# Kernel optimization log

Measured on AMD Instinct MI355X. Metric: run time of the kernel, lower is better.

The kernel has to match this reference:

```python
import jax, jax.numpy as jnp
import numpy as np

NUM_CLASSES = 32
N_ITER = 5
KNN_K = 16


def _inv_softplus(v: float) -> float:
    return float(np.log(np.expm1(v)))


def setup_inputs() -> dict:
    key = jax.random.key(0)
    k1, k2, k3 = jax.random.split(key, 3)
    B, N, C, D = 2, 4096, NUM_CLASSES, 256
    logits = jax.random.normal(k1, (B, N, C), dtype=jnp.float32)
    rois = jax.random.uniform(k2, (B, N, 6), dtype=jnp.float32)
    feats = jax.random.normal(k3, (B, N, D), dtype=jnp.float32)
    raw_sigma = jnp.asarray(_inv_softplus(4.0), dtype=jnp.float32)
    raw_smoothness = jnp.asarray(_inv_softplus(1.0), dtype=jnp.float32)
    return {
        "logits": logits,
        "rois": rois,
        "appearance_features": feats,
        "raw_sigma": raw_sigma,
        "raw_smoothness": raw_smoothness,
    }


def reference(logits, rois, appearance_features, raw_sigma, raw_smoothness):
    B, N, C = logits.shape
    # roi centers of 3D boxes: mean of (xmin,ymin,zmin) and (xmax,ymax,zmax)
    centers = (rois[:, :, :3] + rois[:, :, 3:]) * 0.5
    sq = jnp.sum(centers * centers, axis=-1)  # [B,N]
    dist_sq = jnp.maximum(
        sq[:, :, None] + sq[:, None, :]
        - 2.0 * jnp.einsum("bnd,bmd->bnm", centers, centers),
        0.0,
    )  # squared euclidean [B,N,N]

    identity = jnp.eye(N, dtype=bool)[None]  # [1,N,N]
    valid = jnp.sum(jnp.abs(rois), axis=-1) > 0  # [B,N]
    valid_pairs = valid[:, :, None] & valid[:, None, :]  # [B,N,N]

    # ---- kNN adjacency (symmetric, no self loops) ----
    k_eff = min(KNN_K, max(N - 1, 1))
    masked = jnp.where(valid_pairs & ~identity, dist_sq, jnp.inf)
    neg_topv, knn_idx = jax.lax.top_k(-masked, k_eff)  # smallest k_eff dists
    finite = jnp.isfinite(-neg_topv)  # [B,N,k]
    b_idx = jnp.arange(B)[:, None, None]
    n_idx = jnp.arange(N)[None, :, None]
    adjacency = jnp.zeros((B, N, N), dtype=bool).at[b_idx, n_idx, knn_idx].set(finite)
    adjacency = adjacency | jnp.swapaxes(adjacency, 1, 2)
    adjacency = adjacency & valid_pairs & ~identity

    sigma = jnp.maximum(jax.nn.softplus(raw_sigma), 1e-6)
    smoothness = jax.nn.softplus(raw_smoothness)

    # ---- pairwise kernel: spatial gaussian * appearance cosine affinity ----
    kernel = jnp.exp(-0.5 * dist_sq / (sigma * sigma))
    feat_norm = jnp.maximum(
        jnp.linalg.norm(appearance_features, axis=-1, keepdims=True), 1e-6
    )
    feats_n = appearance_features / feat_norm
    cosine = jnp.einsum("bnd,bmd->bnm", feats_n, feats_n)
    affinity = jnp.clip((cosine + 1.0) * 0.5, 0.0, 1.0)
    kernel = kernel * affinity
    kernel = jnp.where(identity, 0.0, kernel) * adjacency.astype(logits.dtype)
    kernel = kernel / jnp.maximum(jnp.sum(kernel, axis=-1, keepdims=True), 1e-6)

    # ---- class compatibility (normalized squared label distance) ----
    idx = jnp.arange(C, dtype=logits.dtype)
    compat = (idx[:, None] - idx[None, :]) ** 2
    compat = compat / jnp.maximum(compat.max(), 1.0)

    # ---- mean-field iterations ----
    q_probs = jax.nn.softmax(logits, axis=-1)
    refined = logits
    for _ in range(N_ITER):
        q_neighbors = jnp.einsum("bnm,bmc->bnc", kernel, q_probs)
        pairwise_term = jnp.einsum("bnc,cd->bnd", q_neighbors, compat)
        refined = logits - smoothness * pairwise_term
        q_probs = jax.nn.softmax(refined, axis=-1)
    return refined
```

## Files before the change

kernel.cpp:

```cpp
#include <hip/hip_runtime.h>
#include <math.h>

constexpr int B = 2;
constexpr int N = 4096;
constexpr int C = 32;
constexpr int D = 256;
constexpr int K = 16;
constexpr int NW = N / 32;
constexpr int CAP = 128;
constexpr int ROWS = B * N;

__device__ __forceinline__ unsigned short f2bf(float f) {
    unsigned u = __float_as_uint(f);
    return (unsigned short)((u + 0x7fffu + ((u >> 16) & 1u)) >> 16);
}
__device__ __forceinline__ float bflo(unsigned u) { return __uint_as_float(u << 16); }
__device__ __forceinline__ float bfhi(unsigned u) { return __uint_as_float(u & 0xffff0000u); }

__global__ void pre_kernel(const float* __restrict__ rois,
                           const float* __restrict__ feats,
                           float4* __restrict__ centers4,
                           unsigned short* __restrict__ fnbf,
                           uint2* __restrict__ adj_zero) {
    const int t = threadIdx.x;
    const int wid = t >> 6, lane = t & 63;
    const int r = blockIdx.x * 4 + wid;

    adj_zero[blockIdx.x * 256 + t] = make_uint2(0u, 0u);

    if (r >= ROWS) return;

    const float4* f4 = reinterpret_cast<const float4*>(feats) + (size_t)r * (D / 4);
    float4 v = f4[lane];
    float ss = v.x * v.x + v.y * v.y + v.z * v.z + v.w * v.w;
#pragma unroll
    for (int off = 32; off; off >>= 1) ss += __shfl_xor(ss, off);

    const float invn = 1.0f / fmaxf(sqrtf(ss), 1e-6f);
    unsigned u0 = (unsigned)f2bf(v.x * invn) | ((unsigned)f2bf(v.y * invn) << 16);
    unsigned u1 = (unsigned)f2bf(v.z * invn) | ((unsigned)f2bf(v.w * invn) << 16);
    *reinterpret_cast<uint2*>(fnbf + (size_t)r * D + lane * 4) = make_uint2(u0, u1);

    if (lane == 0) {
        const float* rp = rois + (size_t)r * 6;
        float a0 = rp[0], a1 = rp[1], a2 = rp[2], a3 = rp[3], a4 = rp[4], a5 = rp[5];
        float cx = (a0 + a3) * 0.5f, cy = (a1 + a4) * 0.5f, cz = (a2 + a5) * 0.5f;
        float sq = cx * cx + cy * cy + cz * cz;
        float s = fabsf(a0) + fabsf(a1) + fabsf(a2) + fabsf(a3) + fabsf(a4) + fabsf(a5);
        centers4[r] = make_float4(cx, cy, cz, (s > 0.0f) ? sq : INFINITY);
    }
}

__global__ __launch_bounds__(1024, 8) void knn_kernel(const float4* __restrict__ centers4,
                                                      unsigned* __restrict__ adj) {
    __shared__ float4 s_c[N];
    __shared__ unsigned s_pm[16][64];
    __shared__ unsigned long long s_buf[16][64];
    __shared__ int s_cnt[16];
    __shared__ float s_tau[16];

    const int t = threadIdx.x;
    const int lane = t & 63;
    const int wv = t >> 6;
    const int r0 = blockIdx.x * 16;
    const int nbase = r0 & (N - 1);
    const int gbase = r0 - nbase;

    if (t < 16) s_cnt[t] = 0;
    ((unsigned*)s_pm)[t] = 0x7F800000u;
    for (int i = t; i < N; i += 1024) s_c[i] = centers4[gbase + i];
    __syncthreads();

    float4 cmv[4];
    int    mv[4];
#pragma unroll
    for (int u = 0; u < 4; ++u) {
        mv[u] = (wv << 8) + (u << 6) + lane;
        cmv[u] = s_c[mv[u]];
    }

#pragma unroll 4
    for (int rr = 0; rr < 16; ++rr) {
        const int nrow = nbase + rr;
        const float4 rc = s_c[nrow];
        float mn = INFINITY;
#pragma unroll
        for (int u = 0; u < 4; ++u) {
            float dist = fmaxf(rc.w + cmv[u].w -
                               2.0f * (rc.x * cmv[u].x + rc.y * cmv[u].y + rc.z * cmv[u].z), 0.0f);
            mn = fminf(mn, (mv[u] == nrow) ? INFINITY : dist);
        }
        atomicMin(&s_pm[rr][lane], __float_as_uint(mn));
    }
    __syncthreads();

    {
        float v = __uint_as_float(s_pm[wv][lane]);
#pragma unroll
        for (int k = 2; k <= 64; k <<= 1) {
#pragma unroll
            for (int j = k >> 1; j > 0; j >>= 1) {
                float o = __shfl_xor(v, j);
                bool take_min = (((lane & j) == 0) == ((lane & k) == 0));
                v = take_min ? fminf(v, o) : fmaxf(v, o);
            }
        }
        if (lane == 15) s_tau[wv] = v;
    }
    __syncthreads();

#pragma unroll 4
    for (int rr = 0; rr < 16; ++rr) {
        const int nrow = nbase + rr;
        const float tau = s_tau[rr];
        const float4 rc = s_c[nrow];
#pragma unroll
        for (int u = 0; u < 4; ++u) {
            float dist = fmaxf(rc.w + cmv[u].w -
                               2.0f * (rc.x * cmv[u].x + rc.y * cmv[u].y + rc.z * cmv[u].z), 0.0f);
            if (dist <= tau && mv[u] != nrow) {
                int pos = atomicAdd(&s_cnt[rr], 1);
                if (pos < 64)
                    s_buf[rr][pos] = ((unsigned long long)__float_as_uint(dist) << 32)
                                     | (unsigned)mv[u];
            }
        }
    }
    __syncthreads();

    const int rg = r0 + wv;
    const int n = nbase + wv;
    const int cnt = s_cnt[wv];

    int my_sel = -1;
    if (cnt <= 64) {
        unsigned long long key = (lane < cnt) ? s_buf[wv][lane] : ~0ull;
#pragma unroll
        for (int k = 2; k <= 64; k <<= 1) {
#pragma unroll
            for (int j = k >> 1; j > 0; j >>= 1) {
                unsigned long long o = __shfl_xor(key, j);
                bool take_min = (((lane & j) == 0) == ((lane & k) == 0));
                unsigned long long mn = (key < o) ? key : o;
                unsigned long long mx = (key < o) ? o : key;
                key = take_min ? mn : mx;
            }
        }
        if (lane < K && key != ~0ull) my_sel = (int)(unsigned)key;
    } else {
        const float4 cq = s_c[n];
        unsigned long long removed = 0ull;
        for (int round = 0; round < K; ++round) {
            float bd = INFINITY; int bi = 0x7FFFFFFF;
            for (int j = 0; j < 64; ++j) {
                const int m = lane + (j << 6);
                float4 cm = s_c[m];
                float dist = fmaxf(cq.w + cm.w -
                                   2.0f * (cq.x * cm.x + cq.y * cm.y + cq.z * cm.z), 0.0f);
                bool skip = ((removed >> j) & 1ull) || (m == n);
                if (!skip && dist < bd) { bd = dist; bi = m; }
            }
            float md = bd;
#pragma unroll
            for (int off = 32; off; off >>= 1) md = fminf(md, __shfl_xor(md, off));
            if (md == INFINITY) break;
            int kk = (bd == md) ? bi : 0x7FFFFFFF;
#pragma unroll
            for (int off = 32; off; off >>= 1) kk = min(kk, __shfl_xor(kk, off));
            if (lane == round) my_sel = kk;
            if (kk == bi) removed |= 1ull << (bi >> 6);
        }
    }

    if (my_sel >= 0) {
        atomicOr(&adj[(size_t)rg * NW + (my_sel >> 5)], 1u << (my_sel & 31));
        atomicOr(&adj[(size_t)(gbase + my_sel) * NW + (n >> 5)], 1u << (n & 31));
    }
}

__global__ __launch_bounds__(256) void build_kernel(const unsigned short* __restrict__ fnbf,
                             const float4* __restrict__ centers4,
                             const unsigned* __restrict__ adj,
                             uint2* __restrict__ nbr,
                             int* __restrict__ nbr_cnt,
                             const float* __restrict__ raw_sigma,
                             const float* __restrict__ logits,
                             float2* __restrict__ mu0) {
    const int t = threadIdx.x;
    const int lane = t & 63;
    const int wv = t >> 6;
    const int r = blockIdx.x * 4 + wv;
    const int base = r - (r & (N - 1));

    __shared__ float4 s_q[4][16 * 5];
    __shared__ int    s_list[4][CAP];
    __shared__ float  s_w[4][CAP];

    uint2 wpair = *reinterpret_cast<const uint2*>(adj + (size_t)r * NW + 2 * lane);
    const int pc = __popc(wpair.x) + __popc(wpair.y);
    int sc = pc;
#pragma unroll
    for (int off = 1; off < 64; off <<= 1) {
        int o = __shfl_up(sc, off);
        if (lane >= off) sc += o;
    }
    const int total = __shfl(sc, 63);
    const int cnt = total > CAP ? CAP : total;
    int o = sc - pc;
    {
        unsigned ww = wpair.x; int mb = lane * 64;
        while (ww) { int b = __ffs(ww) - 1; if (o < CAP) s_list[wv][o] = mb + b; ++o; ww &= ww - 1; }
        ww = wpair.y; mb = lane * 64 + 32;
        while (ww) { int b = __ffs(ww) - 1; if (o < CAP) s_list[wv][o] = mb + b; ++o; ww &= ww - 1; }
    }

    {
        uint2 qw = *reinterpret_cast<const uint2*>(fnbf + (size_t)r * D + 4 * lane);
        float4 qv = make_float4(bflo(qw.x), bfhi(qw.x), bflo(qw.y), bfhi(qw.y));
        const int e = (lane & 31) >> 1;
        const int s = ((lane >> 5) << 1) | (lane & 1);
        s_q[wv][5 * e + s] = qv;
    }

    const float rs = raw_sigma[0];
    const float sigma = fmaxf(log1pf(expf(rs)), 1e-6f);
    const float nhalf_inv_s2 = -0.5f / (sigma * sigma);
    const float4 cq = centers4[r];
    const uint4* fn4 = reinterpret_cast<const uint4*>(fnbf);

    {
        const int g = lane >> 4;
        const int e = lane & 15;
        for (int i0 = 0; i0 < cnt; i0 += 4) {
            const int i = i0 + g;
            const bool act = (i < cnt);
            const int gm = base + s_list[wv][act ? i : 0];
            uint4 a = fn4[(size_t)gm * 32 + e];
            uint4 b = fn4[(size_t)gm * 32 + 16 + e];
            float4 cm = centers4[gm];
            float4 qa0 = s_q[wv][5 * e + 0], qa1 = s_q[wv][5 * e + 1];
            float4 qb0 = s_q[wv][5 * e + 2], qb1 = s_q[wv][5 * e + 3];
            float p = bflo(a.x) * qa0.x + bfhi(a.x) * qa0.y
                    + bflo(a.y) * qa0.z + bfhi(a.y) * qa0.w
                    + bflo(a.z) * qa1.x + bfhi(a.z) * qa1.y
                    + bflo(a.w) * qa1.z + bfhi(a.w) * qa1.w
                    + bflo(b.x) * qb0.x + bfhi(b.x) * qb0.y
                    + bflo(b.y) * qb0.z + bfhi(b.y) * qb0.w
                    + bflo(b.z) * qb1.x + bfhi(b.z) * qb1.y
                    + bflo(b.w) * qb1.z + bfhi(b.w) * qb1.w;
#pragma unroll
            for (int off = 1; off < 16; off <<= 1) p += __shfl_xor(p, off);
            float aff = fminf(fmaxf((p + 1.0f) * 0.5f, 0.0f), 1.0f);
            float dist = fmaxf(cq.w + cm.w -
                               2.0f * (cq.x * cm.x + cq.y * cm.y + cq.z * cm.z), 0.0f);
            if (e == 0 && act) s_w[wv][i] = expf(dist * nhalf_inv_s2) * aff;
        }
    }

    float ps = 0.0f;
    for (int i = lane; i < cnt; i += 64) ps += s_w[wv][i];
#pragma unroll
    for (int off = 32; off; off >>= 1) ps += __shfl_xor(ps, off);
    const float inv_sum = 1.0f / fmaxf(ps, 1e-6f);

    for (int i = lane; i < cnt; i += 64) {
        nbr[(size_t)r * CAP + i] = make_uint2((unsigned)s_list[wv][i],
                                              __float_as_uint(s_w[wv][i] * inv_sum));
    }
    if (lane == 0) nbr_cnt[r] = cnt;

    if (lane < C) {
        float x = logits[(size_t)r * C + lane];
        float mx = x;
#pragma unroll
        for (int off = 16; off; off >>= 1) mx = fmaxf(mx, __shfl_xor(mx, off, 32));
        float e = expf(x - mx);
        const float fc = (float)lane;
        float s0 = e, s1 = e * fc, s2 = e * fc * fc;
#pragma unroll
        for (int off = 16; off; off >>= 1) {
            s0 += __shfl_xor(s0, off, 32);
            s1 += __shfl_xor(s1, off, 32);
            s2 += __shfl_xor(s2, off, 32);
        }
        if (lane == 0) mu0[r] = make_float2(s1 / s0, s2 / s0);
    }
}

__global__ void iter_kernel(const float* __restrict__ logits,
                            const uint2* __restrict__ nbr,
                            const int* __restrict__ nbr_cnt,
                            const float2* __restrict__ mu_in,
                            float2* __restrict__ mu_out,
                            float* __restrict__ out,
                            const float* __restrict__ raw_smooth,
                            int last) {
    const int t = threadIdx.x;
    const int r = blockIdx.x * 8 + (t >> 5);
    const int c = t & 31;
    const int base = r - (r & (N - 1));
    const float smooth = log1pf(expf(raw_smooth[0]));

    const int cnt = nbr_cnt[r];
    const uint2* np = nbr + (size_t)r * CAP;

    float m0 = 0.0f, m1 = 0.0f, m2 = 0.0f;
    for (int j = c; j < cnt; j += 32) {
        uint2 e = np[j];
        float w = __uint_as_float(e.y);
        float2 mu = mu_in[base + (int)e.x];
        m0 += w;
        m1 += w * mu.x;
        m2 += w * mu.y;
    }
#pragma unroll
    for (int off = 16; off; off >>= 1) {
        m0 += __shfl_xor(m0, off, 32);
        m1 += __shfl_xor(m1, off, 32);
        m2 += __shfl_xor(m2, off, 32);
    }

    const float fc = (float)c;
    float pw = (m2 - 2.0f * fc * m1 + fc * fc * m0) * (1.0f / 961.0f);
    float refined = logits[(size_t)r * C + c] - smooth * pw;

    if (last) {
        out[(size_t)r * C + c] = refined;
        return;
    }

    float mx = refined;
#pragma unroll
    for (int off = 16; off; off >>= 1) mx = fmaxf(mx, __shfl_xor(mx, off, 32));
    float e = expf(refined - mx);
    float s0 = e, s1 = e * fc, s2 = e * fc * fc;
#pragma unroll
    for (int off = 16; off; off >>= 1) {
        s0 += __shfl_xor(s0, off, 32);
        s1 += __shfl_xor(s1, off, 32);
        s2 += __shfl_xor(s2, off, 32);
    }
    if (c == 0) mu_out[r] = make_float2(s1 / s0, s2 / s0);
}

extern "C" void kernel_launch(void* const* d_in, const int* in_sizes, int n_in,
                              void* d_out, int out_size, void* d_ws, size_t ws_size,
                              hipStream_t stream) {
    const float* logits     = (const float*)d_in[0];
    const float* rois       = (const float*)d_in[1];
    const float* feats      = (const float*)d_in[2];
    const float* raw_sigma  = (const float*)d_in[3];
    const float* raw_smooth = (const float*)d_in[4];
    float* out = (float*)d_out;

    char* ws = (char*)d_ws;
    size_t off = 0;
    auto alloc = [&](size_t bytes) -> void* {
        void* p = ws + off;
        off += (bytes + 255) & ~(size_t)255;
        return p;
    };
    float4*         centers4 = (float4*)        alloc((size_t)ROWS * sizeof(float4));
    unsigned short* fnbf     = (unsigned short*)alloc((size_t)ROWS * D * 2);
    unsigned*       adj      = (unsigned*)      alloc((size_t)ROWS * NW * 4);
    uint2*          nbr      = (uint2*)         alloc((size_t)ROWS * CAP * 8);
    int*            nbr_cnt  = (int*)           alloc((size_t)ROWS * 4);
    float2*         mu_a     = (float2*)        alloc((size_t)ROWS * 8);
    float2*         mu_b     = (float2*)        alloc((size_t)ROWS * 8);

    pre_kernel<<<ROWS / 4, 256, 0, stream>>>(rois, feats, centers4, fnbf, (uint2*)adj);
    knn_kernel<<<ROWS / 16, 1024, 0, stream>>>(centers4, adj);
    build_kernel<<<ROWS / 4, 256, 0, stream>>>(fnbf, centers4, adj,
                                               nbr, nbr_cnt, raw_sigma, logits, mu_a);

    float2* mi = mu_a;
    float2* mo = mu_b;
    for (int it = 0; it < 5; ++it) {
        iter_kernel<<<ROWS / 8, 256, 0, stream>>>(logits, nbr, nbr_cnt,
                                                  mi, mo, out, raw_smooth,
                                                  (it == 4) ? 1 : 0);
        float2* tmp = mi; mi = mo; mo = tmp;
    }
}
```

Measured before the change: 71.42 us.

## Fuse pairs of mean-field iterations by recomputing neighbor moments per row

New measurement: 96.44 us. 35.0% more time.

```diff
diff --git a/kernel.cpp b/kernel.cpp
--- a/kernel.cpp
+++ b/kernel.cpp
@@ -287,14 +287,108 @@
     }
 }
 
-__global__ void iter_kernel(const float* __restrict__ logits,
-                            const uint2* __restrict__ nbr,
-                            const int* __restrict__ nbr_cnt,
-                            const float2* __restrict__ mu_in,
-                            float2* __restrict__ mu_out,
-                            float* __restrict__ out,
-                            const float* __restrict__ raw_smooth,
-                            int last) {
+__global__ __launch_bounds__(256) void iter2_kernel(const float* __restrict__ logits,
+                                                    const uint2* __restrict__ nbr,
+                                                    const int* __restrict__ nbr_cnt,
+                                                    const float2* __restrict__ mu_in,
+                                                    float2* __restrict__ mu_out,
+                                                    const float* __restrict__ raw_smooth) {
+    const int t = threadIdx.x;
+    const int lane = t & 63;
+    const int wv = t >> 6;
+    const int r = blockIdx.x * 4 + wv;
+    const int base = r - (r & (N - 1));
+    const float smooth = log1pf(expf(raw_smooth[0]));
+
+    __shared__ float2 s_mu[4][CAP];
+
+    const int cnt = nbr_cnt[r];
+    const uint2* own = nbr + (size_t)r * CAP;
+
+    const int sub = lane & 1;
+    const int p = lane >> 1;
+
+    for (int i0 = 0; i0 < cnt; i0 += 32) {
+        const int i = i0 + p;
+        const bool act = (i < cnt);
+        const int gm = base + (int)own[act ? i : 0].x;
+        const int cm = act ? nbr_cnt[gm] : 0;
+        const uint2* np = nbr + (size_t)gm * CAP;
+
+        float m0 = 0.0f, m1 = 0.0f, m2 = 0.0f;
+        for (int j = sub; j < cm; j += 2) {
+            uint2 e = np[j];
+            float w = __uint_as_float(e.y);
+            float2 mu = mu_in[base + (int)e.x];
+            m0 += w; m1 += w * mu.x; m2 += w * mu.y;
+        }
+        m0 += __shfl_xor(m0, 1); m1 += __shfl_xor(m1, 1); m2 += __shfl_xor(m2, 1);
+
+        const float4* lg4 = reinterpret_cast<const float4*>(logits + (size_t)gm * C + sub * 16);
+        float4 xa = lg4[0], xb = lg4[1], xc = lg4[2], xd = lg4[3];
+        float xv[16] = { xa.x, xa.y, xa.z, xa.w, xb.x, xb.y, xb.z, xb.w,
+                         xc.x, xc.y, xc.z, xc.w, xd.x, xd.y, xd.z, xd.w };
+        float ref[16];
+        float mx = -INFINITY;
+#pragma unroll
+        for (int k = 0; k < 16; ++k) {
+            float fc = (float)(sub * 16 + k);
+            float pw = (m2 - 2.0f * fc * m1 + fc * fc * m0) * (1.0f / 961.0f);
+            float rr = xv[k] - smooth * pw;
+            ref[k] = rr;
+            mx = fmaxf(mx, rr);
+        }
+        mx = fmaxf(mx, __shfl_xor(mx, 1));
+        float s0 = 0.0f, s1 = 0.0f, s2 = 0.0f;
+#pragma unroll
+        for (int k = 0; k < 16; ++k) {
+            float fc = (float)(sub * 16 + k);
+            float e = expf(ref[k] - mx);
+            s0 += e; s1 += e * fc; s2 += e * fc * fc;
+        }
+        s0 += __shfl_xor(s0, 1); s1 += __shfl_xor(s1, 1); s2 += __shfl_xor(s2, 1);
+        if (act && sub == 0) s_mu[wv][i] = make_float2(s1 / s0, s2 / s0);
+    }
+
+    float m0 = 0.0f, m1 = 0.0f, m2 = 0.0f;
+    for (int j = lane; j < cnt; j += 64) {
+        uint2 e = own[j];
+        float w = __uint_as_float(e.y);
+        float2 mu = s_mu[wv][j];
+        m0 += w; m1 += w * mu.x; m2 += w * mu.y;
+    }
+#pragma unroll
+    for (int off = 32; off; off >>= 1) {
+        m0 += __shfl_xor(m0, off);
+        m1 += __shfl_xor(m1, off);
+        m2 += __shfl_xor(m2, off);
+    }
+
+    if (lane < C) {
+        const float fc = (float)lane;
+        float pw = (m2 - 2.0f * fc * m1 + fc * fc * m0) * (1.0f / 961.0f);
+        float refined = logits[(size_t)r * C + lane] - smooth * pw;
+        float mx = refined;
+#pragma unroll
+        for (int off = 16; off; off >>= 1) mx = fmaxf(mx, __shfl_xor(mx, off, 32));
+        float e = expf(refined - mx);
+        float s0 = e, s1 = e * fc, s2 = e * fc * fc;
+#pragma unroll
+        for (int off = 16; off; off >>= 1) {
+            s0 += __shfl_xor(s0, off, 32);
+            s1 += __shfl_xor(s1, off, 32);
+            s2 += __shfl_xor(s2, off, 32);
+        }
+        if (lane == 0) mu_out[r] = make_float2(s1 / s0, s2 / s0);
+    }
+}
+
+__global__ void iter_last_kernel(const float* __restrict__ logits,
+                                 const uint2* __restrict__ nbr,
+                                 const int* __restrict__ nbr_cnt,
+                                 const float2* __restrict__ mu_in,
+                                 float* __restrict__ out,
+                                 const float* __restrict__ raw_smooth) {
     const int t = threadIdx.x;
     const int r = blockIdx.x * 8 + (t >> 5);
     const int c = t & 31;
@@ -309,9 +403,7 @@
         uint2 e = np[j];
         float w = __uint_as_float(e.y);
         float2 mu = mu_in[base + (int)e.x];
-        m0 += w;
-        m1 += w * mu.x;
-        m2 += w * mu.y;
+        m0 += w; m1 += w * mu.x; m2 += w * mu.y;
     }
 #pragma unroll
     for (int off = 16; off; off >>= 1) {
@@ -322,25 +414,7 @@
 
     const float fc = (float)c;
     float pw = (m2 - 2.0f * fc * m1 + fc * fc * m0) * (1.0f / 961.0f);
-    float refined = logits[(size_t)r * C + c] - smooth * pw;
-
-    if (last) {
-        out[(size_t)r * C + c] = refined;
-        return;
-    }
-
-    float mx = refined;
-#pragma unroll
-    for (int off = 16; off; off >>= 1) mx = fmaxf(mx, __shfl_xor(mx, off, 32));
-    float e = expf(refined - mx);
-    float s0 = e, s1 = e * fc, s2 = e * fc * fc;
-#pragma unroll
-    for (int off = 16; off; off >>= 1) {
-        s0 += __shfl_xor(s0, off, 32);
-        s1 += __shfl_xor(s1, off, 32);
-        s2 += __shfl_xor(s2, off, 32);
-    }
-    if (c == 0) mu_out[r] = make_float2(s1 / s0, s2 / s0);
+    out[(size_t)r * C + c] = logits[(size_t)r * C + c] - smooth * pw;
 }
 
 extern "C" void kernel_launch(void* const* d_in, const int* in_sizes, int n_in,
@@ -373,12 +447,7 @@
     build_kernel<<<ROWS / 4, 256, 0, stream>>>(fnbf, centers4, adj,
                                                nbr, nbr_cnt, raw_sigma, logits, mu_a);
 
-    float2* mi = mu_a;
-    float2* mo = mu_b;
-    for (int it = 0; it < 5; ++it) {
-        iter_kernel<<<ROWS / 8, 256, 0, stream>>>(logits, nbr, nbr_cnt,
-                                                  mi, mo, out, raw_smooth,
-                                                  (it == 4) ? 1 : 0);
-        float2* tmp = mi; mi = mo; mo = tmp;
-    }
-}
+    iter2_kernel<<<ROWS / 4, 256, 0, stream>>>(logits, nbr, nbr_cnt, mu_a, mu_b, raw_smooth);
+    iter2_kernel<<<ROWS / 4, 256, 0, stream>>>(logits, nbr, nbr_cnt, mu_b, mu_a, raw_smooth);
+    iter_last_kernel<<<ROWS / 8, 256, 0, stream>>>(logits, nbr, nbr_cnt, mu_a, out, raw_smooth);
+}
```

## Fuse preprocessing into kNN kernel and replace adjacency zeroing with memset

Applied to the files above, without the earlier changes.

New measurement: 74.52 us. 4.3% more time.

```diff
diff --git a/kernel.cpp b/kernel.cpp
--- a/kernel.cpp
+++ b/kernel.cpp
@@ -17,41 +17,12 @@
 __device__ __forceinline__ float bflo(unsigned u) { return __uint_as_float(u << 16); }
 __device__ __forceinline__ float bfhi(unsigned u) { return __uint_as_float(u & 0xffff0000u); }
 
-__global__ void pre_kernel(const float* __restrict__ rois,
-                           const float* __restrict__ feats,
-                           float4* __restrict__ centers4,
-                           unsigned short* __restrict__ fnbf,
-                           uint2* __restrict__ adj_zero) {
-    const int t = threadIdx.x;
-    const int wid = t >> 6, lane = t & 63;
-    const int r = blockIdx.x * 4 + wid;
-
-    adj_zero[blockIdx.x * 256 + t] = make_uint2(0u, 0u);
-
-    if (r >= ROWS) return;
-
-    const float4* f4 = reinterpret_cast<const float4*>(feats) + (size_t)r * (D / 4);
-    float4 v = f4[lane];
-    float ss = v.x * v.x + v.y * v.y + v.z * v.z + v.w * v.w;
-#pragma unroll
-    for (int off = 32; off; off >>= 1) ss += __shfl_xor(ss, off);
-
-    const float invn = 1.0f / fmaxf(sqrtf(ss), 1e-6f);
-    unsigned u0 = (unsigned)f2bf(v.x * invn) | ((unsigned)f2bf(v.y * invn) << 16);
-    unsigned u1 = (unsigned)f2bf(v.z * invn) | ((unsigned)f2bf(v.w * invn) << 16);
-    *reinterpret_cast<uint2*>(fnbf + (size_t)r * D + lane * 4) = make_uint2(u0, u1);
-
-    if (lane == 0) {
-        const float* rp = rois + (size_t)r * 6;
-        float a0 = rp[0], a1 = rp[1], a2 = rp[2], a3 = rp[3], a4 = rp[4], a5 = rp[5];
-        float cx = (a0 + a3) * 0.5f, cy = (a1 + a4) * 0.5f, cz = (a2 + a5) * 0.5f;
-        float sq = cx * cx + cy * cy + cz * cz;
-        float s = fabsf(a0) + fabsf(a1) + fabsf(a2) + fabsf(a3) + fabsf(a4) + fabsf(a5);
-        centers4[r] = make_float4(cx, cy, cz, (s > 0.0f) ? sq : INFINITY);
-    }
-}
-
-__global__ __launch_bounds__(1024, 8) void knn_kernel(const float4* __restrict__ centers4,
+__global__ __launch_bounds__(1024, 8) void knn_kernel(const float* __restrict__ rois,
+                                                      const float* __restrict__ feats,
+                                                      const float* __restrict__ logits,
+                                                      float4* __restrict__ centers4,
+                                                      unsigned short* __restrict__ fnbf,
+                                                      float2* __restrict__ mu0,
                                                       unsigned* __restrict__ adj) {
     __shared__ float4 s_c[N];
     __shared__ unsigned s_pm[16][64];
@@ -65,10 +36,63 @@
     const int r0 = blockIdx.x * 16;
     const int nbase = r0 & (N - 1);
     const int gbase = r0 - nbase;
+    const int rg0 = r0 + wv;
 
     if (t < 16) s_cnt[t] = 0;
     ((unsigned*)s_pm)[t] = 0x7F800000u;
-    for (int i = t; i < N; i += 1024) s_c[i] = centers4[gbase + i];
+
+    {
+        const float4* f4 = reinterpret_cast<const float4*>(feats) + (size_t)rg0 * (D / 4);
+        float4 v = f4[lane];
+        float ss = v.x * v.x + v.y * v.y + v.z * v.z + v.w * v.w;
+#pragma unroll
+        for (int off = 32; off; off >>= 1) ss += __shfl_xor(ss, off);
+        const float invn = 1.0f / fmaxf(sqrtf(ss), 1e-6f);
+        unsigned u0 = (unsigned)f2bf(v.x * invn) | ((unsigned)f2bf(v.y * invn) << 16);
+        unsigned u1 = (unsigned)f2bf(v.z * invn) | ((unsigned)f2bf(v.w * invn) << 16);
+        *reinterpret_cast<uint2*>(fnbf + (size_t)rg0 * D + lane * 4) = make_uint2(u0, u1);
+
+        if (lane < C) {
+            float x = logits[(size_t)rg0 * C + lane];
+            float mx = x;
+#pragma unroll
+            for (int off = 16; off; off >>= 1) mx = fmaxf(mx, __shfl_xor(mx, off, 32));
+            float e = expf(x - mx);
+            const float fc = (float)lane;
+            float s0 = e, s1 = e * fc, s2 = e * fc * fc;
+#pragma unroll
+            for (int off = 16; off; off >>= 1) {
+                s0 += __shfl_xor(s0, off, 32);
+                s1 += __shfl_xor(s1, off, 32);
+                s2 += __shfl_xor(s2, off, 32);
+            }
+            if (lane == 0) mu0[rg0] = make_float2(s1 / s0, s2 / s0);
+        }
+
+        if (lane == 0) {
+            const float* rp = rois + (size_t)rg0 * 6;
+            float a0 = rp[0], a1 = rp[1], a2 = rp[2], a3 = rp[3], a4 = rp[4], a5 = rp[5];
+            float cx = (a0 + a3) * 0.5f, cy = (a1 + a4) * 0.5f, cz = (a2 + a5) * 0.5f;
+            float sq = cx * cx + cy * cy + cz * cz;
+            float s = fabsf(a0) + fabsf(a1) + fabsf(a2) + fabsf(a3) + fabsf(a4) + fabsf(a5);
+            centers4[rg0] = make_float4(cx, cy, cz, (s > 0.0f) ? sq : INFINITY);
+        }
+    }
+
+    {
+        const float2* rois2 = reinterpret_cast<const float2*>(rois);
+        for (int i = t; i < N; i += 1024) {
+            const size_t rb = (size_t)(gbase + i) * 3;
+            float2 p0 = rois2[rb], p1 = rois2[rb + 1], p2 = rois2[rb + 2];
+            float cx = (p0.x + p1.y) * 0.5f;
+            float cy = (p0.y + p2.x) * 0.5f;
+            float cz = (p1.x + p2.y) * 0.5f;
+            float sq = cx * cx + cy * cy + cz * cz;
+            float s = fabsf(p0.x) + fabsf(p0.y) + fabsf(p1.x)
+                    + fabsf(p1.y) + fabsf(p2.x) + fabsf(p2.y);
+            s_c[i] = make_float4(cx, cy, cz, (s > 0.0f) ? sq : INFINITY);
+        }
+    }
     __syncthreads();
 
     float4 cmv[4];
@@ -183,9 +207,7 @@
                              const unsigned* __restrict__ adj,
                              uint2* __restrict__ nbr,
                              int* __restrict__ nbr_cnt,
-                             const float* __restrict__ raw_sigma,
-                             const float* __restrict__ logits,
-                             float2* __restrict__ mu0) {
+                             const float* __restrict__ raw_sigma) {
     const int t = threadIdx.x;
     const int lane = t & 63;
     const int wv = t >> 6;
@@ -268,23 +290,6 @@
                                               __float_as_uint(s_w[wv][i] * inv_sum));
     }
     if (lane == 0) nbr_cnt[r] = cnt;
-
-    if (lane < C) {
-        float x = logits[(size_t)r * C + lane];
-        float mx = x;
-#pragma unroll
-        for (int off = 16; off; off >>= 1) mx = fmaxf(mx, __shfl_xor(mx, off, 32));
-        float e = expf(x - mx);
-        const float fc = (float)lane;
-        float s0 = e, s1 = e * fc, s2 = e * fc * fc;
-#pragma unroll
-        for (int off = 16; off; off >>= 1) {
-            s0 += __shfl_xor(s0, off, 32);
-            s1 += __shfl_xor(s1, off, 32);
-            s2 += __shfl_xor(s2, off, 32);
-        }
-        if (lane == 0) mu0[r] = make_float2(s1 / s0, s2 / s0);
-    }
 }
 
 __global__ void iter_kernel(const float* __restrict__ logits,
@@ -309,9 +314,7 @@
         uint2 e = np[j];
         float w = __uint_as_float(e.y);
         float2 mu = mu_in[base + (int)e.x];
-        m0 += w;
-        m1 += w * mu.x;
-        m2 += w * mu.y;
+        m0 += w; m1 += w * mu.x; m2 += w * mu.y;
     }
 #pragma unroll
     for (int off = 16; off; off >>= 1) {
@@ -368,10 +371,11 @@
     float2*         mu_a     = (float2*)        alloc((size_t)ROWS * 8);
     float2*         mu_b     = (float2*)        alloc((size_t)ROWS * 8);
 
-    pre_kernel<<<ROWS / 4, 256, 0, stream>>>(rois, feats, centers4, fnbf, (uint2*)adj);
-    knn_kernel<<<ROWS / 16, 1024, 0, stream>>>(centers4, adj);
+    hipMemsetAsync(adj, 0, (size_t)ROWS * NW * 4, stream);
+    knn_kernel<<<ROWS / 16, 1024, 0, stream>>>(rois, feats, logits, centers4,
+                                               fnbf, mu_a, adj);
     build_kernel<<<ROWS / 4, 256, 0, stream>>>(fnbf, centers4, adj,
-                                               nbr, nbr_cnt, raw_sigma, logits, mu_a);
+                                               nbr, nbr_cnt, raw_sigma);
 
     float2* mi = mu_a;
     float2* mo = mu_b;
```
